# Optimization experiments

Hardware: AMD Instinct MI355X
Metric: run time of the kernel (lower is better)

Reference implementation:

```python
import jax, jax.numpy as jnp
import numpy as np

DIM = 192
HEADS = 6
WS = 7        # window_size
SS = 3        # shift_size
MLP_RATIO = 4.0
B = 64
H_RES = 56
W_RES = 56
EPS = 1e-5


def _rel_index(ws):
    # standard Swin relative position index, (ws*ws, ws*ws) int
    coords = np.stack(np.meshgrid(np.arange(ws), np.arange(ws), indexing='ij'))  # 2,ws,ws
    flat = coords.reshape(2, -1)                                                 # 2,N
    rel = (flat[:, :, None] - flat[:, None, :]).transpose(1, 2, 0)               # N,N,2
    rel[:, :, 0] += ws - 1
    rel[:, :, 1] += ws - 1
    rel[:, :, 0] *= 2 * ws - 1
    return rel.sum(-1)  # N,N


def _attn_mask(H, W, ws, ss):
    # (num_windows, N, N) float mask with 0 / -100, static given H,W,ws,ss
    img = np.zeros((H, W))
    sl = (slice(0, -ws), slice(-ws, -ss), slice(-ss, None))
    cnt = 0
    for hs in sl:
        for wsl in sl:
            img[hs, wsl] = cnt
            cnt += 1
    mw = img.reshape(H // ws, ws, W // ws, ws).transpose(0, 2, 1, 3).reshape(-1, ws * ws)
    diff = mw[:, None, :] - mw[:, :, None]
    return jnp.asarray(np.where(diff != 0, -100.0, 0.0).astype(np.float32))


def _ln(x, g, b):
    mu = x.mean(-1, keepdims=True)
    var = jnp.var(x, axis=-1, keepdims=True)
    return (x - mu) * jax.lax.rsqrt(var + EPS) * g + b


def setup_inputs() -> dict:
    key = jax.random.key(0)
    ks = jax.random.split(key, 8)
    C = DIM
    hid = int(C * MLP_RATIO)
    nrm = lambda k, s: jax.random.normal(k, s, jnp.float32) * 0.02
    return {
        "x": jax.random.normal(ks[0], (B, H_RES * W_RES, C), jnp.float32),
        "norm1_g": jnp.ones((C,), jnp.float32),
        "norm1_b": jnp.zeros((C,), jnp.float32),
        "qkv_w": nrm(ks[1], (3 * C, C)),
        "qkv_b": jnp.zeros((3 * C,), jnp.float32),
        "rel_bias_table": nrm(ks[2], ((2 * WS - 1) ** 2, HEADS)),
        "proj_w": nrm(ks[3], (C, C)),
        "proj_b": jnp.zeros((C,), jnp.float32),
        "norm2_g": jnp.ones((C,), jnp.float32),
        "norm2_b": jnp.zeros((C,), jnp.float32),
        "fc1_w": nrm(ks[4], (hid, C)),
        "fc1_b": jnp.zeros((hid,), jnp.float32),
        "fc2_w": nrm(ks[5], (C, hid)),
        "fc2_b": jnp.zeros((C,), jnp.float32),
        "H": H_RES,
        "W": W_RES,
    }


def _block(x, norm1_g, norm1_b, qkv_w, qkv_b, rel_bias_table, proj_w, proj_b,
           norm2_g, norm2_b, fc1_w, fc1_b, fc2_w, fc2_b, H, W):
    Bn, L, C = x.shape
    ws = min(WS, H, W)
    ss = SS if ws > SS else 0
    nH, nW = H // ws, W // ws
    N = ws * ws
    hd = C // HEADS

    shortcut = x
    h = _ln(x, norm1_g, norm1_b).reshape(Bn, H, W, C)
    if ss > 0:
        h = jnp.roll(h, (-ss, -ss), axis=(1, 2))
    # window partition -> (Bn*nH*nW, N, C)
    win = h.reshape(Bn, nH, ws, nW, ws, C).transpose(0, 1, 3, 2, 4, 5).reshape(-1, N, C)

    qkv = win @ qkv_w.T + qkv_b                       # (nWin, N, 3C)
    qkv = qkv.reshape(-1, N, 3, HEADS, hd).transpose(2, 0, 3, 1, 4)
    q, k, v = qkv[0], qkv[1], qkv[2]                  # (nWin, heads, N, hd)
    scale = float(hd) ** -0.5
    attn = jnp.einsum('whnd,whmd->whnm', q * scale, k)

    idx = _rel_index(ws)                              # N,N (static)
    bias = rel_bias_table[idx.reshape(-1)].reshape(N, N, HEADS).transpose(2, 0, 1)
    attn = attn + bias[None]

    if ss > 0:
        mask = _attn_mask(H, W, ws, ss)               # (nH*nW, N, N)
        attn = attn.reshape(Bn, nH * nW, HEADS, N, N) + mask[None, :, None]
        attn = attn.reshape(-1, HEADS, N, N)

    attn = jax.nn.softmax(attn, axis=-1)
    out = jnp.einsum('whnm,whmd->whnd', attn, v)      # (nWin, heads, N, hd)
    out = out.transpose(0, 2, 1, 3).reshape(-1, N, C)
    out = out @ proj_w.T + proj_b

    # window reverse -> (Bn, H, W, C)
    out = out.reshape(Bn, nH, nW, ws, ws, C).transpose(0, 1, 3, 2, 4, 5).reshape(Bn, H, W, C)
    if ss > 0:
        out = jnp.roll(out, (ss, ss), axis=(1, 2))
    x = shortcut + out.reshape(Bn, H * W, C)

    h2 = _ln(x, norm2_g, norm2_b)
    h2 = jax.nn.gelu(h2 @ fc1_w.T + fc1_b, approximate=False)
    h2 = h2 @ fc2_w.T + fc2_b
    return x + h2


def reference(x, norm1_g, norm1_b, qkv_w, qkv_b, rel_bias_table, proj_w, proj_b,
              norm2_g, norm2_b, fc1_w, fc1_b, fc2_w, fc2_b, H, W):
    return _block(x, norm1_g, norm1_b, qkv_w, qkv_b, rel_bias_table, proj_w, proj_b,
                  norm2_g, norm2_b, fc1_w, fc1_b, fc2_w, fc2_b, H, W)
```

## Files before the change

kernel.cpp:

```cpp
#include <hip/hip_runtime.h>
#include <hip/hip_bf16.h>
#include <math.h>

typedef __attribute__((ext_vector_type(8))) short short8;
typedef __attribute__((ext_vector_type(4))) float floatx4;

__device__ __forceinline__ float bf2f(unsigned short u) {
    union { unsigned int i; float f; } v;
    v.i = ((unsigned int)u) << 16;
    return v.f;
}
__device__ __forceinline__ unsigned short f2bf(float f) {
    union { float f; unsigned int i; } v;
    v.f = f;
    return (unsigned short)((v.i + 0x7FFFu + ((v.i >> 16) & 1u)) >> 16);
}
__device__ __forceinline__ void async16(const void* g, void* l) {
    __builtin_amdgcn_global_load_lds((const __attribute__((address_space(1))) void*)g,
                                     (__attribute__((address_space(3))) void*)l, 16, 0, 0);
}

__global__ __launch_bounds__(256) void cvt_kernel(const float* __restrict__ s,
                                                  unsigned short* __restrict__ d, int n,
                                                  int cut, float scale) {
    int i = blockIdx.x * 256 + threadIdx.x;
    if (i < n) d[i] = f2bf(s[i] * (i < cut ? scale : 1.0f));
}
__global__ __launch_bounds__(256) void biasscale_kernel(const float* __restrict__ s,
                                                        float* __restrict__ d, int n,
                                                        int cut, float scale) {
    int i = blockIdx.x * 256 + threadIdx.x;
    if (i < n) d[i] = s[i] * (i < cut ? scale : 1.0f);
}

__global__ __launch_bounds__(256) void zerov_kernel(unsigned short* __restrict__ vT) {
    int idx = blockIdx.x * 256 + threadIdx.x;
    size_t row = (size_t)(idx >> 1);
    uint4 z = make_uint4(0u, 0u, 0u, 0u);
    *(uint4*)(vT + row * 64 + 48 + (idx & 1) * 8) = z;
}

__global__ __launch_bounds__(256) void bmt_kernel(const float* __restrict__ btab,
                                                  float* __restrict__ tbl) {
    int idx = blockIdx.x * 256 + threadIdx.x;
    int key = idx & 63;
    int q = (idx >> 6) & 63;
    int h = (idx >> 12) % 6;
    int cls = idx / (4096 * 6);
    float v;
    if (key >= 49) v = -3.0e38f;
    else if (q >= 49) v = 0.0f;
    else {
        int qi = q / 7, qj = q % 7, ki = key / 7, kj = key % 7;
        v = btab[((qi - ki + 6) * 13 + (qj - kj + 6)) * 6 + h];
        int whT = (cls >> 1) & 1, wwT = cls & 1;
        int rq = (whT ? (qi < 4 ? 1 : 2) : 0) * 3 + (wwT ? (qj < 4 ? 1 : 2) : 0);
        int rk = (whT ? (ki < 4 ? 1 : 2) : 0) * 3 + (wwT ? (kj < 4 ? 1 : 2) : 0);
        if (rq != rk) v -= 100.0f;
    }
    tbl[idx] = v;
}

__global__ __launch_bounds__(256) void ln_kernel(const float* __restrict__ src,
                                                 const float* __restrict__ gw,
                                                 const float* __restrict__ bw,
                                                 unsigned short* __restrict__ dst,
                                                 int mode) {
    int o = blockIdx.x * 4 + (threadIdx.x >> 6);
    int lane = threadIdx.x & 63;
    size_t srow;
    if (mode == 0) {
        int win = o / 49, n = o % 49;
        int b = win >> 6, wl = win & 63;
        int wh = wl >> 3, ww = wl & 7;
        int i = n / 7, j = n % 7;
        int pr = (wh * 7 + i + 3) % 56;
        int pc = (ww * 7 + j + 3) % 56;
        srow = ((size_t)b * 3136 + (size_t)(pr * 56 + pc)) * 192;
    } else {
        srow = (size_t)o * 192;
    }
    float v0 = src[srow + lane];
    float v1 = src[srow + lane + 64];
    float v2 = src[srow + lane + 128];
    float s = v0 + v1 + v2;
    float s2 = v0 * v0 + v1 * v1 + v2 * v2;
    #pragma unroll
    for (int off = 32; off > 0; off >>= 1) {
        s += __shfl_xor(s, off);
        s2 += __shfl_xor(s2, off);
    }
    float mean = s * (1.0f / 192.0f);
    float var = s2 * (1.0f / 192.0f) - mean * mean;
    float inv = rsqrtf(var + 1e-5f);
    size_t drow = (size_t)o * 192;
    dst[drow + lane]       = f2bf((v0 - mean) * inv * gw[lane]       + bw[lane]);
    dst[drow + lane + 64]  = f2bf((v1 - mean) * inv * gw[lane + 64]  + bw[lane + 64]);
    dst[drow + lane + 128] = f2bf((v2 - mean) * inv * gw[lane + 128] + bw[lane + 128]);
}

template <int EPI>
__global__ __launch_bounds__(256) void gemm_nt(const unsigned short* __restrict__ A,
                                               const unsigned short* __restrict__ W,
                                               const float* __restrict__ bias,
                                               int K, int ldo, int mbase, int gx, int noff,
                                               unsigned short* __restrict__ outb,
                                               float* __restrict__ outf,
                                               const float* __restrict__ resid) {
    __shared__ __align__(16) unsigned short Al[2][128][32];
    __shared__ __align__(16) unsigned short Wl[2][64][32];
    int tid = threadIdx.x;
    int lane = tid & 63;
    int wv = tid >> 6;
    int wm = wv >> 1, wn = wv & 1;
    int bid = blockIdx.x;
    int swz = (bid & 7) * ((int)gridDim.x >> 3) + (bid >> 3);
    int bx = swz % gx, by = swz / gx;
    int m0 = by * 128;
    int n0 = bx * 64;
    int quad = lane >> 4, l15 = lane & 15;

    int srow = lane >> 2;
    int scol = (lane & 3) * 8;
    const unsigned short* aP0 = A + (size_t)(m0 + wv * 32 + srow) * K + scol;
    const unsigned short* aP1 = aP0 + (size_t)16 * K;
    const unsigned short* wP  = W + (size_t)(noff + n0 + wv * 16 + srow) * K + scol;

    floatx4 acc[4][2];
    floatx4 zero = {0.f, 0.f, 0.f, 0.f};
    #pragma unroll
    for (int a = 0; a < 4; ++a)
        #pragma unroll
        for (int b = 0; b < 2; ++b) acc[a][b] = zero;

    async16(aP0, &Al[0][wv * 32][0]);
    async16(aP1, &Al[0][wv * 32 + 16][0]);
    async16(wP,  &Wl[0][wv * 16][0]);
    __syncthreads();

    int nsteps = K >> 5;
    int cur = 0;
    for (int t = 0; t < nsteps; ++t) {
        if (t + 1 < nsteps) {
            int kt = (t + 1) << 5;
            int nb = cur ^ 1;
            async16(aP0 + kt, &Al[nb][wv * 32][0]);
            async16(aP1 + kt, &Al[nb][wv * 32 + 16][0]);
            async16(wP + kt,  &Wl[nb][wv * 16][0]);
        }
        short8 af[4], wf[2];
        #pragma unroll
        for (int mt = 0; mt < 4; ++mt)
            af[mt] = *(const short8*)&Al[cur][wm * 64 + mt * 16 + l15][quad * 8];
        #pragma unroll
        for (int nt = 0; nt < 2; ++nt)
            wf[nt] = *(const short8*)&Wl[cur][wn * 32 + nt * 16 + l15][quad * 8];
        #pragma unroll
        for (int mt = 0; mt < 4; ++mt)
            #pragma unroll
            for (int nt = 0; nt < 2; ++nt)
                acc[mt][nt] = __builtin_amdgcn_mfma_f32_16x16x32_bf16(af[mt], wf[nt], acc[mt][nt], 0, 0, 0);
        __syncthreads();
        cur ^= 1;
    }

    #pragma unroll
    for (int mt = 0; mt < 4; ++mt) {
        #pragma unroll
        for (int nt = 0; nt < 2; ++nt) {
            if (EPI == 4) {
                int nv = n0 + wn * 32 + nt * 16 + l15;
                int hh = nv >> 5, dd = nv & 31;
                float bv = bias[384 + nv];
                int mq = m0 + wm * 64 + mt * 16 + quad * 4;
                int w = mq / 49, key0 = mq - w * 49;
                unsigned short* vrow = outb + ((size_t)(w * 6 + hh) * 32 + dd) * 64;
                #pragma unroll
                for (int r = 0; r < 4; ++r) {
                    int key = key0 + r;
                    unsigned short* dp = vrow + (key >= 49 ? key - 49 + 12288 : key);
                    *dp = f2bf(acc[mt][nt][r] + bv);
                }
            } else {
                #pragma unroll
                for (int r = 0; r < 4; ++r) {
                    int m = m0 + wm * 64 + mt * 16 + quad * 4 + r;
                    int n = n0 + wn * 32 + nt * 16 + l15;
                    float v = acc[mt][nt][r] + bias[n];
                    if (EPI == 0) {
                        outb[(size_t)m * ldo + n] = f2bf(v);
                    } else if (EPI == 1) {
                        float g = 0.5f * v * (1.0f + erff(v * 0.70710678118654752f));
                        outb[(size_t)m * ldo + n] = f2bf(g);
                    } else if (EPI == 2) {
                        int win = m / 49, np = m % 49;
                        int b = win >> 6, wl = win & 63;
                        int wh = wl >> 3, ww = wl & 7;
                        int i = np / 7, j = np % 7;
                        int pr = (wh * 7 + i + 3) % 56;
                        int pc = (ww * 7 + j + 3) % 56;
                        size_t dst = ((size_t)b * 3136 + (size_t)(pr * 56 + pc)) * 192 + n;
                        outf[dst] = resid[dst] + v;
                    } else {
                        size_t dst = (size_t)(mbase + m) * ldo + n;
                        outf[dst] = resid[dst] + v;
                    }
                }
            }
        }
    }
}

__global__ __launch_bounds__(192) void attn_kernel(const unsigned short* __restrict__ qkv,
                                                   const unsigned short* __restrict__ vT,
                                                   const float* __restrict__ tbl,
                                                   unsigned short* __restrict__ awin) {
    __shared__ __align__(16) unsigned short Pb[3][64][72];
    int w = blockIdx.x >> 1;
    int hb = (blockIdx.x & 1) * 3;
    int hl = threadIdx.x >> 6;
    int h = hb + hl;
    int lane = threadIdx.x & 63;
    int quad = lane >> 4, l15 = lane & 15;
    const unsigned short* base = qkv + (size_t)w * 49 * 576;
    int wl = w & 63;
    int cls = ((wl >> 3) == 7 ? 2 : 0) + ((wl & 7) == 7 ? 1 : 0);
    const float* tb = tbl + (size_t)(cls * 6 + h) * 4096;

    short8 kf[4], qf[4];
    #pragma unroll
    for (int mt = 0; mt < 4; ++mt)
        kf[mt] = *(const short8*)(base + (size_t)(mt * 16 + l15) * 576 + 192 + h * 32 + quad * 8);
    #pragma unroll
    for (int nt = 0; nt < 4; ++nt)
        qf[nt] = *(const short8*)(base + (size_t)(nt * 16 + l15) * 576 + h * 32 + quad * 8);

    const unsigned short* vb = vT + (size_t)(w * 6 + h) * 2048;
    short8 vf[2][2];
    #pragma unroll
    for (int ks = 0; ks < 2; ++ks)
        #pragma unroll
        for (int nt = 0; nt < 2; ++nt)
            vf[ks][nt] = *(const short8*)(vb + (size_t)(nt * 16 + l15) * 64 + ks * 32 + quad * 8);

    floatx4 S[4][4];
    #pragma unroll
    for (int mt = 0; mt < 4; ++mt)
        #pragma unroll
        for (int nt = 0; nt < 4; ++nt) {
            floatx4 cinit = *(const floatx4*)(tb + (nt * 16 + l15) * 64 + mt * 16 + quad * 4);
            S[mt][nt] = __builtin_amdgcn_mfma_f32_16x16x32_bf16(kf[mt], qf[nt], cinit, 0, 0, 0);
        }

    #pragma unroll
    for (int mt = 0; mt < 4; ++mt)
        #pragma unroll
        for (int nt = 0; nt < 4; ++nt)
            #pragma unroll
            for (int rr = 0; rr < 4; ++rr)
                S[mt][nt][rr] = __expf(S[mt][nt][rr]);

    float rinv[4];
    #pragma unroll
    for (int nt = 0; nt < 4; ++nt) {
        float s = 0.f;
        #pragma unroll
        for (int mt = 0; mt < 4; ++mt)
            s += (S[mt][nt][0] + S[mt][nt][1]) + (S[mt][nt][2] + S[mt][nt][3]);
        s += __shfl_xor(s, 16);
        s += __shfl_xor(s, 32);
        rinv[nt] = 1.0f / s;
    }

    #pragma unroll
    for (int mt = 0; mt < 4; ++mt) {
        #pragma unroll
        for (int nt = 0; nt < 4; ++nt) {
            __hip_bfloat162 p0 = __float22bfloat162_rn(
                make_float2(S[mt][nt][0] * rinv[nt], S[mt][nt][1] * rinv[nt]));
            __hip_bfloat162 p1 = __float22bfloat162_rn(
                make_float2(S[mt][nt][2] * rinv[nt], S[mt][nt][3] * rinv[nt]));
            union { __hip_bfloat162 h2[2]; uint2 u; } pk;
            pk.h2[0] = p0;
            pk.h2[1] = p1;
            *(uint2*)&Pb[hl][nt * 16 + l15][mt * 16 + quad * 4] = pk.u;
        }
    }

    floatx4 O[4][2];
    floatx4 zero = {0.f, 0.f, 0.f, 0.f};
    #pragma unroll
    for (int mt = 0; mt < 4; ++mt)
        #pragma unroll
        for (int nt = 0; nt < 2; ++nt) O[mt][nt] = zero;
    #pragma unroll
    for (int ks = 0; ks < 2; ++ks) {
        #pragma unroll
        for (int mt = 0; mt < 4; ++mt) {
            short8 pf = *(const short8*)&Pb[hl][mt * 16 + l15][ks * 32 + quad * 8];
            #pragma unroll
            for (int nt = 0; nt < 2; ++nt)
                O[mt][nt] = __builtin_amdgcn_mfma_f32_16x16x32_bf16(pf, vf[ks][nt], O[mt][nt], 0, 0, 0);
        }
    }
    #pragma unroll
    for (int mt = 0; mt < 4; ++mt) {
        #pragma unroll
        for (int rr = 0; rr < 4; ++rr) {
            int q = mt * 16 + quad * 4 + rr;
            if (q < 49) {
                #pragma unroll
                for (int nt = 0; nt < 2; ++nt)
                    awin[((size_t)w * 49 + q) * 192 + h * 32 + nt * 16 + l15] =
                        f2bf(O[mt][nt][rr]);
            }
        }
    }
}

extern "C" void kernel_launch(void* const* d_in, const int* in_sizes, int n_in,
                              void* d_out, int out_size, void* d_ws, size_t ws_size,
                              hipStream_t stream) {
    const float* x      = (const float*)d_in[0];
    const float* n1g    = (const float*)d_in[1];
    const float* n1b    = (const float*)d_in[2];
    const float* qkv_w  = (const float*)d_in[3];
    const float* qkv_b  = (const float*)d_in[4];
    const float* btab   = (const float*)d_in[5];
    const float* proj_w = (const float*)d_in[6];
    const float* proj_b = (const float*)d_in[7];
    const float* n2g    = (const float*)d_in[8];
    const float* n2b    = (const float*)d_in[9];
    const float* fc1_w  = (const float*)d_in[10];
    const float* fc1_b  = (const float*)d_in[11];
    const float* fc2_w  = (const float*)d_in[12];
    const float* fc2_b  = (const float*)d_in[13];
    float* out = (float*)d_out;

    char* p = (char*)d_ws;
    size_t off = 0;
    auto alloc = [&](size_t bytes) {
        char* r = p + off;
        off = (off + bytes + 255) & ~(size_t)255;
        return r;
    };
    unsigned short* wq   = (unsigned short*)alloc((size_t)576 * 192 * 2);
    unsigned short* wp   = (unsigned short*)alloc((size_t)192 * 192 * 2);
    unsigned short* w1   = (unsigned short*)alloc((size_t)768 * 192 * 2);
    unsigned short* w2   = (unsigned short*)alloc((size_t)192 * 768 * 2);
    unsigned short* hwin = (unsigned short*)alloc((size_t)200704 * 192 * 2);
    unsigned short* qkvb = (unsigned short*)alloc((size_t)200704 * 576 * 2);
    float*          xres = (float*)alloc((size_t)200704 * 192 * 4);
    unsigned short* g1   = (unsigned short*)alloc((size_t)50176 * 768 * 2);
    if (ws_size < off) return;
    float* tbl   = (float*)g1;
    float* qkvbs = (float*)g1 + 98304;
    unsigned short* vT = (unsigned short*)xres;

    const float scale = 0.17677669529663687f;
    cvt_kernel<<<432, 256, 0, stream>>>(qkv_w, wq, 110592, 36864, scale);
    cvt_kernel<<<144, 256, 0, stream>>>(proj_w, wp, 36864, 0, 1.0f);
    cvt_kernel<<<576, 256, 0, stream>>>(fc1_w, w1, 147456, 0, 1.0f);
    cvt_kernel<<<576, 256, 0, stream>>>(fc2_w, w2, 147456, 0, 1.0f);
    biasscale_kernel<<<3, 256, 0, stream>>>(qkv_b, qkvbs, 576, 192, scale);
    bmt_kernel<<<384, 256, 0, stream>>>(btab, tbl);
    zerov_kernel<<<6144, 256, 0, stream>>>(vT);

    ln_kernel<<<50176, 256, 0, stream>>>(x, n1g, n1b, hwin, 0);
    gemm_nt<0><<<9408, 256, 0, stream>>>(hwin, wq, qkvbs, 192, 576, 0, 6, 0,
                                         qkvb, nullptr, nullptr);
    gemm_nt<4><<<4704, 256, 0, stream>>>(hwin, wq, qkvbs, 192, 0, 0, 3, 384,
                                         vT, nullptr, nullptr);
    attn_kernel<<<8192, 192, 0, stream>>>(qkvb, vT, tbl, hwin );
    gemm_nt<2><<<4704, 256, 0, stream>>>(hwin, wp, proj_b, 192, 192, 0, 3, 0,
                                         nullptr, xres, x);
    unsigned short* h2 = qkvb;
    ln_kernel<<<50176, 256, 0, stream>>>(xres, n2g, n2b, h2, 1);
    for (int c = 0; c < 4; ++c) {
        int mb = c * 50176;
        gemm_nt<1><<<4704, 256, 0, stream>>>(h2 + (size_t)mb * 192, w1, fc1_b, 192, 768, 0,
                                             12, 0, g1, nullptr, nullptr);
        gemm_nt<3><<<1176, 256, 0, stream>>>(g1, w2, fc2_b, 768, 192, mb, 3, 0,
                                             nullptr, out, xres);
    }
}
```

Measured before the change: 1.158 ms.

## Widen GEMM N-tiles, swizzle LDS layout, and split barrier/waitcnt pipelining

Makes the GEMM N-tile width a template parameter (128 or 192 columns) so each block reuses its A tile across more output columns, and shrinks the launch grids to match. It also XOR-swizzles the LDS column layout to cut bank conflicts, and replaces __syncthreads with explicit vmcnt/lgkmcnt waits and s_barrier so the next stage's loads overlap compute. The wider tiles raise register and LDS use, which can lower occupancy, and the smaller grids (for example 392 blocks for fc2) may underfill the GPU.

```diff
diff --git a/kernel.cpp b/kernel.cpp
--- a/kernel.cpp
+++ b/kernel.cpp
@@ -99,7 +99,7 @@
     dst[drow + lane + 128] = f2bf((v2 - mean) * inv * gw[lane + 128] + bw[lane + 128]);
 }
 
-template <int EPI>
+template <int EPI, int NT>
 __global__ __launch_bounds__(256) void gemm_nt(const unsigned short* __restrict__ A,
                                                const unsigned short* __restrict__ W,
                                                const float* __restrict__ bias,
@@ -108,7 +108,8 @@
                                                float* __restrict__ outf,
                                                const float* __restrict__ resid) {
     __shared__ __align__(16) unsigned short Al[2][128][32];
-    __shared__ __align__(16) unsigned short Wl[2][64][32];
+    __shared__ __align__(16) unsigned short Bl[2][NT * 32][32];
+    constexpr int NL = 2 + NT / 2;
     int tid = threadIdx.x;
     int lane = tid & 63;
     int wv = tid >> 6;
@@ -117,59 +118,64 @@
     int swz = (bid & 7) * ((int)gridDim.x >> 3) + (bid >> 3);
     int bx = swz % gx, by = swz / gx;
     int m0 = by * 128;
-    int n0 = bx * 64;
+    int n0 = bx * (NT * 32);
     int quad = lane >> 4, l15 = lane & 15;
 
     int srow = lane >> 2;
-    int scol = (lane & 3) * 8;
-    const unsigned short* aP0 = A + (size_t)(m0 + wv * 32 + srow) * K + scol;
-    const unsigned short* aP1 = aP0 + (size_t)16 * K;
-    const unsigned short* wP  = W + (size_t)(noff + n0 + wv * 16 + srow) * K + scol;
-
-    floatx4 acc[4][2];
+    int scol = ((lane & 3) ^ (srow & 3)) * 8;
+    const unsigned short* aP = A + (size_t)(m0 + wv * 32 + srow) * K + scol;
+    const unsigned short* wP = W + (size_t)(noff + n0 + wv * NT * 8 + srow) * K + scol;
+
+    floatx4 acc[4][NT];
     floatx4 zero = {0.f, 0.f, 0.f, 0.f};
     #pragma unroll
     for (int a = 0; a < 4; ++a)
         #pragma unroll
-        for (int b = 0; b < 2; ++b) acc[a][b] = zero;
-
-    async16(aP0, &Al[0][wv * 32][0]);
-    async16(aP1, &Al[0][wv * 32 + 16][0]);
-    async16(wP,  &Wl[0][wv * 16][0]);
-    __syncthreads();
-
-    int nsteps = K >> 5;
-    int cur = 0;
-    for (int t = 0; t < nsteps; ++t) {
-        if (t + 1 < nsteps) {
-            int kt = (t + 1) << 5;
-            int nb = cur ^ 1;
-            async16(aP0 + kt, &Al[nb][wv * 32][0]);
-            async16(aP1 + kt, &Al[nb][wv * 32 + 16][0]);
-            async16(wP + kt,  &Wl[nb][wv * 16][0]);
-        }
-        short8 af[4], wf[2];
+        for (int b = 0; b < NT; ++b) acc[a][b] = zero;
+
+    auto stage = [&](int b, int kt) {
+        async16(aP + kt, &Al[b][wv * 32][0]);
+        async16(aP + (size_t)16 * K + kt, &Al[b][wv * 32 + 16][0]);
+        #pragma unroll
+        for (int c = 0; c < NT / 2; ++c)
+            async16(wP + (size_t)(c * 16) * K + kt, &Bl[b][wv * NT * 8 + c * 16][0]);
+    };
+
+    stage(0, 0);
+    int ns = K >> 5;
+    int rc = (quad ^ (l15 & 3)) * 8;
+    for (int t = 0; t < ns; ++t) {
+        int cur = t & 1;
+        if (t + 1 < ns) {
+            stage(cur ^ 1, (t + 1) << 5);
+            asm volatile("s_waitcnt vmcnt(%0)" ::"n"(NL) : "memory");
+        } else {
+            asm volatile("s_waitcnt vmcnt(0)" ::: "memory");
+        }
+        __builtin_amdgcn_s_barrier();
+        short8 af[4], wf[NT];
         #pragma unroll
         for (int mt = 0; mt < 4; ++mt)
-            af[mt] = *(const short8*)&Al[cur][wm * 64 + mt * 16 + l15][quad * 8];
-        #pragma unroll
-        for (int nt = 0; nt < 2; ++nt)
-            wf[nt] = *(const short8*)&Wl[cur][wn * 32 + nt * 16 + l15][quad * 8];
+            af[mt] = *(const short8*)&Al[cur][wm * 64 + mt * 16 + l15][rc];
+        #pragma unroll
+        for (int nt = 0; nt < NT; ++nt)
+            wf[nt] = *(const short8*)&Bl[cur][wn * NT * 16 + nt * 16 + l15][rc];
+        asm volatile("s_waitcnt lgkmcnt(0)" ::: "memory");
+        __builtin_amdgcn_sched_barrier(0);
+        __builtin_amdgcn_s_barrier();
         #pragma unroll
         for (int mt = 0; mt < 4; ++mt)
             #pragma unroll
-            for (int nt = 0; nt < 2; ++nt)
+            for (int nt = 0; nt < NT; ++nt)
                 acc[mt][nt] = __builtin_amdgcn_mfma_f32_16x16x32_bf16(af[mt], wf[nt], acc[mt][nt], 0, 0, 0);
-        __syncthreads();
-        cur ^= 1;
     }
 
     #pragma unroll
     for (int mt = 0; mt < 4; ++mt) {
         #pragma unroll
-        for (int nt = 0; nt < 2; ++nt) {
+        for (int nt = 0; nt < NT; ++nt) {
             if (EPI == 4) {
-                int nv = n0 + wn * 32 + nt * 16 + l15;
+                int nv = n0 + wn * NT * 16 + nt * 16 + l15;
                 int hh = nv >> 5, dd = nv & 31;
                 float bv = bias[384 + nv];
                 int mq = m0 + wm * 64 + mt * 16 + quad * 4;
@@ -185,7 +191,7 @@
                 #pragma unroll
                 for (int r = 0; r < 4; ++r) {
                     int m = m0 + wm * 64 + mt * 16 + quad * 4 + r;
-                    int n = n0 + wn * 32 + nt * 16 + l15;
+                    int n = n0 + wn * NT * 16 + nt * 16 + l15;
                     float v = acc[mt][nt][r] + bias[n];
                     if (EPI == 0) {
                         outb[(size_t)m * ldo + n] = f2bf(v);
@@ -367,20 +373,20 @@
     zerov_kernel<<<6144, 256, 0, stream>>>(vT);
 
     ln_kernel<<<50176, 256, 0, stream>>>(x, n1g, n1b, hwin, 0);
-    gemm_nt<0><<<9408, 256, 0, stream>>>(hwin, wq, qkvbs, 192, 576, 0, 6, 0,
-                                         qkvb, nullptr, nullptr);
-    gemm_nt<4><<<4704, 256, 0, stream>>>(hwin, wq, qkvbs, 192, 0, 0, 3, 384,
-                                         vT, nullptr, nullptr);
+    gemm_nt<0, 4><<<4704, 256, 0, stream>>>(hwin, wq, qkvbs, 192, 576, 0, 3, 0,
+                                            qkvb, nullptr, nullptr);
+    gemm_nt<4, 6><<<1568, 256, 0, stream>>>(hwin, wq, qkvbs, 192, 0, 0, 1, 384,
+                                            vT, nullptr, nullptr);
     attn_kernel<<<8192, 192, 0, stream>>>(qkvb, vT, tbl, hwin );
-    gemm_nt<2><<<4704, 256, 0, stream>>>(hwin, wp, proj_b, 192, 192, 0, 3, 0,
-                                         nullptr, xres, x);
+    gemm_nt<2, 6><<<1568, 256, 0, stream>>>(hwin, wp, proj_b, 192, 192, 0, 1, 0,
+                                            nullptr, xres, x);
     unsigned short* h2 = qkvb;
     ln_kernel<<<50176, 256, 0, stream>>>(xres, n2g, n2b, h2, 1);
     for (int c = 0; c < 4; ++c) {
         int mb = c * 50176;
-        gemm_nt<1><<<4704, 256, 0, stream>>>(h2 + (size_t)mb * 192, w1, fc1_b, 192, 768, 0,
-                                             12, 0, g1, nullptr, nullptr);
-        gemm_nt<3><<<1176, 256, 0, stream>>>(g1, w2, fc2_b, 768, 192, mb, 3, 0,
-                                             nullptr, out, xres);
-    }
-}
+        gemm_nt<1, 4><<<2352, 256, 0, stream>>>(h2 + (size_t)mb * 192, w1, fc1_b, 192, 768, 0,
+                                                6, 0, g1, nullptr, nullptr);
+        gemm_nt<3, 6><<<392, 256, 0, stream>>>(g1, w2, fc2_b, 768, 192, mb, 1, 0,
+                                               nullptr, out, xres);
+    }
+}
```

New measurement: 1.211 ms. +4.5%, slower.
